# Optimization experiments

Hardware: AMD Instinct MI355X
Metric: run time of the kernel (lower is better)

The kernel has to match this reference:

```python
import jax, jax.numpy as jnp
import numpy as np

DIM = 512

def setup_inputs() -> dict:
    key = jax.random.key(0)
    ks = jax.random.split(key, 8)
    B, T, S, D = 4, 128, 512, DIM
    scale = 1.0 / np.sqrt(D)
    return {
        "inp": jax.random.normal(ks[0], (B, T, D), jnp.float32),
        "context": jax.random.normal(ks[1], (B, S, D), jnp.float32),
        # linear_query: Linear(D, D, bias=True)
        "Wq": jax.random.normal(ks[2], (D, D), jnp.float32) * scale,
        "bq": jax.random.normal(ks[3], (D,), jnp.float32) * scale,
        # linear_context: Linear(D, D, bias=False)
        "Wc": jax.random.normal(ks[4], (D, D), jnp.float32) * scale,
        # v: Linear(D, 1, bias=False)
        "v": jax.random.normal(ks[5], (D,), jnp.float32) * scale,
        # linear_out: Linear(2D, D, bias=True)
        "Wout": jax.random.normal(ks[6], (D, 2 * D), jnp.float32) * scale,
        "bout": jax.random.normal(ks[7], (D,), jnp.float32) * scale,
    }

def reference(inp, context, Wq, bq, Wc, v, Wout, bout):
    # inp: (B,T,D) target queries; context: (B,S,D) source states
    wq = jnp.einsum('btd,ed->bte', inp, Wq) + bq          # (B,T,D)
    uh = jnp.einsum('bsd,ed->bse', context, Wc)            # (B,S,D)
    # additive (Bahdanau) score: v^T tanh(Wq q_t + Wc h_s)
    wquh = jnp.tanh(wq[:, :, None, :] + uh[:, None, :, :])  # (B,T,S,D)
    align = jnp.einsum('btsd,d->bts', wquh, v)             # (B,T,S)
    align_vectors = jax.nn.softmax(align, axis=-1)          # softmax over src_len
    c = jnp.einsum('bts,bsd->btd', align_vectors, context)  # context vector
    concat_c = jnp.concatenate([c, inp], axis=-1)           # (B,T,2D)
    attn_h = jnp.einsum('btf,ef->bte', concat_c, Wout) + bout  # (B,T,D)
    return attn_h, align_vectors
```

## Files before the change

kernel.cpp:

```cpp
#include <hip/hip_runtime.h>
#include <hip/hip_bf16.h>
#include <math.h>


typedef __attribute__((ext_vector_type(8))) short short8;
typedef __attribute__((ext_vector_type(4))) float f32x4;
typedef unsigned short ushort_t;

static __device__ __forceinline__ unsigned short f2bf(float x) {
    union { __hip_bfloat16 h; unsigned short u; } c;
    c.h = __float2bfloat16(x);
    return c.u;
}
static __device__ __forceinline__ int bf2x(float lo, float hi) {
    return (int)(((unsigned)f2bf(hi) << 16) | (unsigned)f2bf(lo));
}

template<bool BF>
static __device__ __forceinline__ void load16(const void* base, size_t elemoff,
                                              int4& r0, int4& r1) {
    if (BF) {
        const int4* p = (const int4*)((const ushort_t*)base + elemoff);
        r0 = p[0]; r1 = p[1];
    } else {
        const float4* p = (const float4*)((const float*)base + elemoff);
        float4 a = p[0], b = p[1], c = p[2], d = p[3];
        r0.x = bf2x(a.x, a.y); r0.y = bf2x(a.z, a.w);
        r0.z = bf2x(b.x, b.y); r0.w = bf2x(b.z, b.w);
        r1.x = bf2x(c.x, c.y); r1.y = bf2x(c.z, c.w);
        r1.z = bf2x(d.x, d.y); r1.w = bf2x(d.z, d.w);
    }
}

template<bool A_BF, bool W_BF, int EPI>
static __device__ __forceinline__ void gemm_body(
    ushort_t* As, ushort_t* Ws,
    const void* A, const void* W, const float* bias, const float* partial,
    void* Cv, int K, int lda, int ldw, int ldc, int bm, int bn)
{
    const int tid = threadIdx.x;
    const int wave = tid >> 6, lane = tid & 63;
    const int mh = (wave & 1) * 32, nh = (wave >> 1) * 32;
    const int quad = lane >> 4, l16 = lane & 15;
    const int srow = tid >> 2, schunk = tid & 3;

    const size_t aoff = (size_t)(bm + srow) * lda + schunk * 16;
    const size_t woff = (size_t)(bn + srow) * ldw + schunk * 16;
    int4* AsW = (int4*)&As[srow * 72 + schunk * 16];
    int4* WsW = (int4*)&Ws[srow * 72 + schunk * 16];

    f32x4 acc00 = {0.f, 0.f, 0.f, 0.f}, acc01 = acc00, acc10 = acc00, acc11 = acc00;

    int4 a0r, a1r, w0r, w1r;
    load16<A_BF>(A, aoff, a0r, a1r);
    load16<W_BF>(W, woff, w0r, w1r);

    for (int k0 = 0; k0 < K; k0 += 64) {
        AsW[0] = a0r; AsW[1] = a1r;
        WsW[0] = w0r; WsW[1] = w1r;
        __syncthreads();
        if (k0 + 64 < K) {
            load16<A_BF>(A, aoff + k0 + 64, a0r, a1r);
            load16<W_BF>(W, woff + k0 + 64, w0r, w1r);
        }
        #pragma unroll
        for (int kk = 0; kk < 64; kk += 32) {
            short8 a0 = *(const short8*)&As[(mh + l16) * 72 + kk + quad * 8];
            short8 a1 = *(const short8*)&As[(mh + 16 + l16) * 72 + kk + quad * 8];
            short8 b0 = *(const short8*)&Ws[(nh + l16) * 72 + kk + quad * 8];
            short8 b1 = *(const short8*)&Ws[(nh + 16 + l16) * 72 + kk + quad * 8];
            acc00 = __builtin_amdgcn_mfma_f32_16x16x32_bf16(a0, b0, acc00, 0, 0, 0);
            acc01 = __builtin_amdgcn_mfma_f32_16x16x32_bf16(a0, b1, acc01, 0, 0, 0);
            acc10 = __builtin_amdgcn_mfma_f32_16x16x32_bf16(a1, b0, acc10, 0, 0, 0);
            acc11 = __builtin_amdgcn_mfma_f32_16x16x32_bf16(a1, b1, acc11, 0, 0, 0);
        }
        __syncthreads();
    }

    const int col0 = bn + nh + l16;
    const int col1 = col0 + 16;
    float bias0 = bias ? bias[col0] : 0.f;
    float bias1 = bias ? bias[col1] : 0.f;

    f32x4 accs[2][2] = {{acc00, acc01}, {acc10, acc11}};
    #pragma unroll
    for (int mt = 0; mt < 2; ++mt) {
        #pragma unroll
        for (int r = 0; r < 4; ++r) {
            int row = bm + mh + mt * 16 + quad * 4 + r;
            size_t rowoff = (size_t)row * ldc;
            float v0 = accs[mt][0][r] + bias0;
            float v1 = accs[mt][1][r] + bias1;
            if (EPI == 1) { v0 = __expf(2.f * v0); v1 = __expf(2.f * v1); }
            if (EPI == 3) { v0 += partial[rowoff + col0]; v1 += partial[rowoff + col1]; }
            if (EPI == 2) {
                ushort_t* C = (ushort_t*)Cv;
                C[rowoff + col0] = f2bf(v0);
                C[rowoff + col1] = f2bf(v1);
            } else {
                float* C = (float*)Cv;
                C[rowoff + col0] = v0;
                C[rowoff + col1] = v1;
            }
        }
    }
}

__global__ __launch_bounds__(256) void fused_front(
    const float* __restrict__ inp, const float* __restrict__ ctx,
    const float* __restrict__ Wq, const float* __restrict__ bq,
    const float* __restrict__ Wc, const float* __restrict__ Wout,
    const float* __restrict__ bout,
    float* __restrict__ Ew, float* __restrict__ Eu, float* __restrict__ Y0,
    ushort_t* __restrict__ GT)
{
    __shared__ ushort_t As[64 * 72];
    __shared__ ushort_t Ws[64 * 72];
    const int bid = blockIdx.x;

    if (bid < 64) {
        gemm_body<false, false, 1>(As, Ws, inp, Wq, bq, nullptr, Ew,
                                   512, 512, 512, 512, (bid & 7) * 64, (bid >> 3) * 64);
    } else if (bid < 320) {
        int i = bid - 64;
        gemm_body<false, false, 1>(As, Ws, ctx, Wc, nullptr, nullptr, Eu,
                                   512, 512, 512, 512, (i & 31) * 64, (i >> 5) * 64);
    } else if (bid < 576) {
        int i = bid - 320;
        int b = i >> 6, j = i & 63;
        gemm_body<false, false, 2>(As, Ws, Wout, ctx + (size_t)b * 262144, nullptr,
                                   nullptr, GT + (size_t)b * 262144,
                                   512, 1024, 512, 512, (j & 7) * 64, (j >> 3) * 64);
    } else {
        int i = bid - 576;
        gemm_body<false, false, 0>(As, Ws, inp, Wout + 512, bout, nullptr, Y0,
                                   512, 512, 1024, 512, (i & 7) * 64, (i >> 3) * 64);
    }
}

__global__ __launch_bounds__(256) void align_kernel(
    const float* __restrict__ Ew, const float* __restrict__ Eu,
    const float* __restrict__ v, float* __restrict__ out)
{
    const int lane = threadIdx.x & 63, wave = threadIdx.x >> 6;
    const int b = blockIdx.z;
    const int t0 = blockIdx.y * 16 + wave * 4;
    const int s0 = blockIdx.x * 8;

    const float* wp = Ew + (((size_t)(b * 128 + t0)) << 9);
    const float* up = Eu + (((size_t)(b * 512 + s0)) << 9);

    float acc[4][8];
    #pragma unroll
    for (int i = 0; i < 4; ++i)
        #pragma unroll
        for (int j = 0; j < 8; ++j) acc[i][j] = 0.f;
    float vsum = 0.f;

    for (int k0 = 0; k0 < 512; k0 += 64) {
        float vk = v[k0 + lane];
        vsum += vk;
        float w0 = wp[k0 + lane];
        float w1 = wp[512 + k0 + lane];
        float w2 = wp[1024 + k0 + lane];
        float w3 = wp[1536 + k0 + lane];
        #pragma unroll
        for (int j = 0; j < 8; ++j) {
            float u = up[((size_t)j << 9) + k0 + lane];
            float d0 = fmaf(w0, u, 1.f);
            float d1 = fmaf(w1, u, 1.f);
            float d2 = fmaf(w2, u, 1.f);
            float d3 = fmaf(w3, u, 1.f);
            float r0 = __builtin_amdgcn_rcpf(d0);
            float r1 = __builtin_amdgcn_rcpf(d1);
            float r2 = __builtin_amdgcn_rcpf(d2);
            float r3 = __builtin_amdgcn_rcpf(d3);
            acc[0][j] = fmaf(vk, r0, acc[0][j]);
            acc[1][j] = fmaf(vk, r1, acc[1][j]);
            acc[2][j] = fmaf(vk, r2, acc[2][j]);
            acc[3][j] = fmaf(vk, r3, acc[3][j]);
        }
    }

    float V = vsum;
    #pragma unroll
    for (int off = 32; off; off >>= 1) V += __shfl_xor(V, off, 64);

    float r0 = 0.f, r1 = 0.f, r2 = 0.f, r3 = 0.f;
    #pragma unroll
    for (int j = 0; j < 8; ++j) {
        float a0 = acc[0][j], a1 = acc[1][j], a2 = acc[2][j], a3 = acc[3][j];
        #pragma unroll
        for (int off = 32; off; off >>= 1) {
            a0 += __shfl_xor(a0, off, 64);
            a1 += __shfl_xor(a1, off, 64);
            a2 += __shfl_xor(a2, off, 64);
            a3 += __shfl_xor(a3, off, 64);
        }
        if (lane == j) {
            r0 = fmaf(-2.f, a0, V);
            r1 = fmaf(-2.f, a1, V);
            r2 = fmaf(-2.f, a2, V);
            r3 = fmaf(-2.f, a3, V);
        }
    }
    if (lane < 8) {
        size_t o = (((size_t)(b * 128 + t0)) << 9) + s0 + lane;
        out[o] = r0;
        out[o + 512] = r1;
        out[o + 1024] = r2;
        out[o + 1536] = r3;
    }
}

__global__ __launch_bounds__(256) void softmax_512(
    const float* __restrict__ Sraw, float* __restrict__ alignv,
    ushort_t* __restrict__ pbf)
{
    const int row = blockIdx.x;
    const float* p = Sraw + ((size_t)row << 9);
    float* a = alignv + ((size_t)row << 9);
    ushort_t* q = pbf + ((size_t)row << 9);
    const int tid = threadIdx.x;
    float x0 = p[tid];
    float x1 = p[tid + 256];

    float m = fmaxf(x0, x1);
    #pragma unroll
    for (int off = 32; off > 0; off >>= 1)
        m = fmaxf(m, __shfl_xor(m, off, 64));
    __shared__ float redm[4];
    __shared__ float reds[4];
    const int wave = tid >> 6;
    if ((tid & 63) == 0) redm[wave] = m;
    __syncthreads();
    m = fmaxf(fmaxf(redm[0], redm[1]), fmaxf(redm[2], redm[3]));

    float e0 = __expf(x0 - m);
    float e1 = __expf(x1 - m);
    float s = e0 + e1;
    #pragma unroll
    for (int off = 32; off > 0; off >>= 1)
        s += __shfl_xor(s, off, 64);
    if ((tid & 63) == 0) reds[wave] = s;
    __syncthreads();
    s = reds[0] + reds[1] + reds[2] + reds[3];
    float r = 1.0f / s;
    float p0 = e0 * r, p1 = e1 * r;
    a[tid] = p0;
    a[tid + 256] = p1;
    q[tid] = f2bf(p0);
    q[tid + 256] = f2bf(p1);
}

__global__ __launch_bounds__(256) void gemm_att(
    const ushort_t* __restrict__ P, const ushort_t* __restrict__ GT,
    const float* __restrict__ Y0, float* __restrict__ attn)
{
    __shared__ ushort_t As[64 * 72];
    __shared__ ushort_t Ws[64 * 72];
    const int b = blockIdx.z;
    gemm_body<true, true, 3>(As, Ws,
                             P + (size_t)b * 65536, GT + (size_t)b * 262144,
                             nullptr, Y0 + (size_t)b * 65536,
                             attn + (size_t)b * 65536,
                             512, 512, 512, 512, blockIdx.x * 64, blockIdx.y * 64);
}

extern "C" void kernel_launch(void* const* d_in, const int* in_sizes, int n_in,
                              void* d_out, int out_size, void* d_ws, size_t ws_size,
                              hipStream_t stream)
{
    const float* inp  = (const float*)d_in[0];
    const float* ctx  = (const float*)d_in[1];
    const float* Wq   = (const float*)d_in[2];
    const float* bq   = (const float*)d_in[3];
    const float* Wc   = (const float*)d_in[4];
    const float* v    = (const float*)d_in[5];
    const float* Wout = (const float*)d_in[6];
    const float* bout = (const float*)d_in[7];

    float* out    = (float*)d_out;
    float* attn   = out;
    float* alignv = out + 262144;

    float* ws = (float*)d_ws;
    float* Ew   = ws;
    float* Eu   = ws + 262144;
    float* Y0   = ws + 1310720;
    float* Sraw = ws + 1572864;
    ushort_t* GT   = (ushort_t*)(ws + 1835008);
    ushort_t* P_bf = (ushort_t*)(ws + 2359296);

    fused_front<<<dim3(640), 256, 0, stream>>>(inp, ctx, Wq, bq, Wc, Wout, bout,
                                               Ew, Eu, Y0, GT);
    align_kernel<<<dim3(64, 8, 4), 256, 0, stream>>>(Ew, Eu, v, Sraw);
    softmax_512<<<dim3(512), 256, 0, stream>>>(Sraw, alignv, P_bf);
    gemm_att<<<dim3(2, 8, 4), 256, 0, stream>>>(P_bf, GT, Y0, attn);
}
```

Baseline: 119.7 us.

## Fuse softmax into align and final GEMM using unnormalized exp with atomic row sums

Removes the separate softmax kernel. The align kernel now writes exp(score) directly and atomically adds per-row sums, with no max subtraction, which is safe because |score| is bounded by sum|v| via tanh. The final GEMM scales its A rows by 1/rowsum while loading and converting to bf16, and the blockIdx.y==0 blocks also write the normalized align vectors. This saves one launch and a round-trip of the score matrix, at the cost of atomics, an extra zeroing block in the front kernel, and fp32 reads of E instead of bf16 reads in the GEMM.

```diff
diff --git a/kernel.cpp b/kernel.cpp
--- a/kernel.cpp
+++ b/kernel.cpp
@@ -32,11 +32,26 @@
     }
 }
 
-template<bool A_BF, bool W_BF, int EPI>
+static __device__ __forceinline__ void load16s(const void* base, size_t elemoff,
+                                               float s, int4& r0, int4& r1) {
+    const float4* p = (const float4*)((const float*)base + elemoff);
+    float4 a = p[0], b = p[1], c = p[2], d = p[3];
+    a.x *= s; a.y *= s; a.z *= s; a.w *= s;
+    b.x *= s; b.y *= s; b.z *= s; b.w *= s;
+    c.x *= s; c.y *= s; c.z *= s; c.w *= s;
+    d.x *= s; d.y *= s; d.z *= s; d.w *= s;
+    r0.x = bf2x(a.x, a.y); r0.y = bf2x(a.z, a.w);
+    r0.z = bf2x(b.x, b.y); r0.w = bf2x(b.z, b.w);
+    r1.x = bf2x(c.x, c.y); r1.y = bf2x(c.z, c.w);
+    r1.z = bf2x(d.x, d.y); r1.w = bf2x(d.z, d.w);
+}
+
+template<bool A_BF, bool W_BF, int EPI, bool A_SCALE = false>
 static __device__ __forceinline__ void gemm_body(
     ushort_t* As, ushort_t* Ws,
     const void* A, const void* W, const float* bias, const float* partial,
-    void* Cv, int K, int lda, int ldw, int ldc, int bm, int bn)
+    void* Cv, int K, int lda, int ldw, int ldc, int bm, int bn,
+    const float* ascale = nullptr)
 {
     const int tid = threadIdx.x;
     const int wave = tid >> 6, lane = tid & 63;
@@ -49,10 +64,13 @@
     int4* AsW = (int4*)&As[srow * 72 + schunk * 16];
     int4* WsW = (int4*)&Ws[srow * 72 + schunk * 16];
 
+    const float asc = A_SCALE ? ascale[srow] : 1.f;
+
     f32x4 acc00 = {0.f, 0.f, 0.f, 0.f}, acc01 = acc00, acc10 = acc00, acc11 = acc00;
 
     int4 a0r, a1r, w0r, w1r;
-    load16<A_BF>(A, aoff, a0r, a1r);
+    if (A_SCALE) load16s(A, aoff, asc, a0r, a1r);
+    else         load16<A_BF>(A, aoff, a0r, a1r);
     load16<W_BF>(W, woff, w0r, w1r);
 
     for (int k0 = 0; k0 < K; k0 += 64) {
@@ -60,7 +78,8 @@
         WsW[0] = w0r; WsW[1] = w1r;
         __syncthreads();
         if (k0 + 64 < K) {
-            load16<A_BF>(A, aoff + k0 + 64, a0r, a1r);
+            if (A_SCALE) load16s(A, aoff + k0 + 64, asc, a0r, a1r);
+            else         load16<A_BF>(A, aoff + k0 + 64, a0r, a1r);
             load16<W_BF>(W, woff + k0 + 64, w0r, w1r);
         }
         #pragma unroll
@@ -112,11 +131,18 @@
     const float* __restrict__ Wc, const float* __restrict__ Wout,
     const float* __restrict__ bout,
     float* __restrict__ Ew, float* __restrict__ Eu, float* __restrict__ Y0,
-    ushort_t* __restrict__ GT)
+    ushort_t* __restrict__ GT, float* __restrict__ rowsum)
 {
     __shared__ ushort_t As[64 * 72];
     __shared__ ushort_t Ws[64 * 72];
     const int bid = blockIdx.x;
+
+    if (bid >= 640) {
+        float4 z = {0.f, 0.f, 0.f, 0.f};
+        ((float4*)rowsum)[threadIdx.x * 2]     = z;
+        ((float4*)rowsum)[threadIdx.x * 2 + 1] = z;
+        return;
+    }
 
     if (bid < 64) {
         gemm_body<false, false, 1>(As, Ws, inp, Wq, bq, nullptr, Ew,
@@ -138,9 +164,10 @@
     }
 }
 
-__global__ __launch_bounds__(256) void align_kernel(
+__global__ __launch_bounds__(256) void align_exp(
     const float* __restrict__ Ew, const float* __restrict__ Eu,
-    const float* __restrict__ v, float* __restrict__ out)
+    const float* __restrict__ v, float* __restrict__ out,
+    float* __restrict__ rowsum)
 {
     const int lane = threadIdx.x & 63, wave = threadIdx.x >> 6;
     const int b = blockIdx.z;
@@ -204,67 +231,65 @@
             r3 = fmaf(-2.f, a3, V);
         }
     }
+
+    float e0 = 0.f, e1 = 0.f, e2 = 0.f, e3 = 0.f;
     if (lane < 8) {
+        e0 = __expf(r0); e1 = __expf(r1); e2 = __expf(r2); e3 = __expf(r3);
         size_t o = (((size_t)(b * 128 + t0)) << 9) + s0 + lane;
-        out[o] = r0;
-        out[o + 512] = r1;
-        out[o + 1024] = r2;
-        out[o + 1536] = r3;
-    }
-}
-
-__global__ __launch_bounds__(256) void softmax_512(
-    const float* __restrict__ Sraw, float* __restrict__ alignv,
-    ushort_t* __restrict__ pbf)
-{
-    const int row = blockIdx.x;
-    const float* p = Sraw + ((size_t)row << 9);
-    float* a = alignv + ((size_t)row << 9);
-    ushort_t* q = pbf + ((size_t)row << 9);
-    const int tid = threadIdx.x;
-    float x0 = p[tid];
-    float x1 = p[tid + 256];
-
-    float m = fmaxf(x0, x1);
-    #pragma unroll
-    for (int off = 32; off > 0; off >>= 1)
-        m = fmaxf(m, __shfl_xor(m, off, 64));
-    __shared__ float redm[4];
-    __shared__ float reds[4];
-    const int wave = tid >> 6;
-    if ((tid & 63) == 0) redm[wave] = m;
-    __syncthreads();
-    m = fmaxf(fmaxf(redm[0], redm[1]), fmaxf(redm[2], redm[3]));
-
-    float e0 = __expf(x0 - m);
-    float e1 = __expf(x1 - m);
-    float s = e0 + e1;
-    #pragma unroll
-    for (int off = 32; off > 0; off >>= 1)
-        s += __shfl_xor(s, off, 64);
-    if ((tid & 63) == 0) reds[wave] = s;
-    __syncthreads();
-    s = reds[0] + reds[1] + reds[2] + reds[3];
-    float r = 1.0f / s;
-    float p0 = e0 * r, p1 = e1 * r;
-    a[tid] = p0;
-    a[tid + 256] = p1;
-    q[tid] = f2bf(p0);
-    q[tid + 256] = f2bf(p1);
-}
-
-__global__ __launch_bounds__(256) void gemm_att(
-    const ushort_t* __restrict__ P, const ushort_t* __restrict__ GT,
-    const float* __restrict__ Y0, float* __restrict__ attn)
+        out[o] = e0;
+        out[o + 512] = e1;
+        out[o + 1024] = e2;
+        out[o + 1536] = e3;
+    }
+    #pragma unroll
+    for (int off = 4; off; off >>= 1) {
+        e0 += __shfl_xor(e0, off, 64);
+        e1 += __shfl_xor(e1, off, 64);
+        e2 += __shfl_xor(e2, off, 64);
+        e3 += __shfl_xor(e3, off, 64);
+    }
+    if (lane == 0) {
+        const int row = b * 128 + t0;
+        atomicAdd(&rowsum[row],     e0);
+        atomicAdd(&rowsum[row + 1], e1);
+        atomicAdd(&rowsum[row + 2], e2);
+        atomicAdd(&rowsum[row + 3], e3);
+    }
+}
+
+__global__ __launch_bounds__(256) void gemm_att_sm(
+    const float* __restrict__ E, const ushort_t* __restrict__ GT,
+    const float* __restrict__ Y0, const float* __restrict__ rowsum,
+    float* __restrict__ attn, float* __restrict__ alignv)
 {
     __shared__ ushort_t As[64 * 72];
     __shared__ ushort_t Ws[64 * 72];
+    __shared__ float rinv[64];
     const int b = blockIdx.z;
-    gemm_body<true, true, 3>(As, Ws,
-                             P + (size_t)b * 65536, GT + (size_t)b * 262144,
-                             nullptr, Y0 + (size_t)b * 65536,
-                             attn + (size_t)b * 65536,
-                             512, 512, 512, 512, blockIdx.x * 64, blockIdx.y * 64);
+    const int bm = blockIdx.x * 64;
+    const int tid = threadIdx.x;
+
+    if (tid < 64) rinv[tid] = 1.0f / rowsum[b * 128 + bm + tid];
+    __syncthreads();
+
+    gemm_body<false, true, 3, true>(As, Ws,
+                                    E + (size_t)b * 65536, GT + (size_t)b * 262144,
+                                    nullptr, Y0 + (size_t)b * 65536,
+                                    attn + (size_t)b * 65536,
+                                    512, 512, 512, 512, bm, blockIdx.y * 64, rinv);
+
+    if (blockIdx.y == 0) {
+        const float* Eb = E + (size_t)b * 65536;
+        float* av = alignv + (size_t)b * 65536;
+        for (int i = tid; i < 8192; i += 256) {
+            int r = i >> 7, c4 = i & 127;
+            const float4* src = (const float4*)(Eb + ((size_t)(bm + r) << 9));
+            float4 e = src[c4];
+            float s = rinv[r];
+            e.x *= s; e.y *= s; e.z *= s; e.w *= s;
+            ((float4*)(av + ((size_t)(bm + r) << 9)))[c4] = e;
+        }
+    }
 }
 
 extern "C" void kernel_launch(void* const* d_in, const int* in_sizes, int n_in,
@@ -288,13 +313,12 @@
     float* Ew   = ws;
     float* Eu   = ws + 262144;
     float* Y0   = ws + 1310720;
-    float* Sraw = ws + 1572864;
-    ushort_t* GT   = (ushort_t*)(ws + 1835008);
-    ushort_t* P_bf = (ushort_t*)(ws + 2359296);
-
-    fused_front<<<dim3(640), 256, 0, stream>>>(inp, ctx, Wq, bq, Wc, Wout, bout,
-                                               Ew, Eu, Y0, GT);
-    align_kernel<<<dim3(64, 8, 4), 256, 0, stream>>>(Ew, Eu, v, Sraw);
-    softmax_512<<<dim3(512), 256, 0, stream>>>(Sraw, alignv, P_bf);
-    gemm_att<<<dim3(2, 8, 4), 256, 0, stream>>>(P_bf, GT, Y0, attn);
-}
+    float* E    = ws + 1572864;
+    ushort_t* GT = (ushort_t*)(ws + 1835008);
+    float* rowsum = ws + 2359296;
+
+    fused_front<<<dim3(641), 256, 0, stream>>>(inp, ctx, Wq, bq, Wc, Wout, bout,
+                                               Ew, Eu, Y0, GT, rowsum);
+    align_exp<<<dim3(64, 8, 4), 256, 0, stream>>>(Ew, Eu, v, E, rowsum);
+    gemm_att_sm<<<dim3(2, 8, 4), 256, 0, stream>>>(E, GT, Y0, rowsum, attn, alignv);
+}
```

Result: slower. 173.0 us (+44.6%).

## Transpose context projection and pair reciprocals in align kernel

Applied to the files above, without the earlier changes.

The context projection is now written transposed (EuT, laid out [b][d][s]) so that in the align kernel each lane owns one source position and reads along s with coalesced loads. This removes the per-row cross-lane shuffle reductions. Terms are combined two at a time as (v0*B+v1*A)/(A*B), which halves the number of reciprocal instructions at the cost of a few extra multiplies. Risks include overflow or precision loss from multiplying denominators, and the Ew and v loads are now lane-uniform.

```diff
diff --git a/kernel.cpp b/kernel.cpp
--- a/kernel.cpp
+++ b/kernel.cpp
@@ -111,7 +111,7 @@
     const float* __restrict__ Wq, const float* __restrict__ bq,
     const float* __restrict__ Wc, const float* __restrict__ Wout,
     const float* __restrict__ bout,
-    float* __restrict__ Ew, float* __restrict__ Eu, float* __restrict__ Y0,
+    float* __restrict__ Ew, float* __restrict__ EuT, float* __restrict__ Y0,
     ushort_t* __restrict__ GT)
 {
     __shared__ ushort_t As[64 * 72];
@@ -123,8 +123,10 @@
                                    512, 512, 512, 512, (bid & 7) * 64, (bid >> 3) * 64);
     } else if (bid < 320) {
         int i = bid - 64;
-        gemm_body<false, false, 1>(As, Ws, ctx, Wc, nullptr, nullptr, Eu,
-                                   512, 512, 512, 512, (i & 31) * 64, (i >> 5) * 64);
+        int b = i >> 6, j = i & 63;
+        gemm_body<false, false, 1>(As, Ws, Wc, ctx + (size_t)b * 262144, nullptr,
+                                   nullptr, EuT + (size_t)b * 262144,
+                                   512, 512, 512, 512, (j & 7) * 64, (j >> 3) * 64);
     } else if (bid < 576) {
         int i = bid - 320;
         int b = i >> 6, j = i & 63;
@@ -139,78 +141,56 @@
 }
 
 __global__ __launch_bounds__(256) void align_kernel(
-    const float* __restrict__ Ew, const float* __restrict__ Eu,
+    const float* __restrict__ Ew, const float* __restrict__ EuT,
     const float* __restrict__ v, float* __restrict__ out)
 {
     const int lane = threadIdx.x & 63, wave = threadIdx.x >> 6;
     const int b = blockIdx.z;
-    const int t0 = blockIdx.y * 16 + wave * 4;
-    const int s0 = blockIdx.x * 8;
-
-    const float* wp = Ew + (((size_t)(b * 128 + t0)) << 9);
-    const float* up = Eu + (((size_t)(b * 512 + s0)) << 9);
-
-    float acc[4][8];
-    #pragma unroll
-    for (int i = 0; i < 4; ++i)
+    const int t = blockIdx.y * 4 + wave;
+    const int s = blockIdx.x * 64 + lane;
+
+    const float* wp = Ew + (((size_t)(b * 128 + t)) << 9);
+    const float* up = EuT + ((size_t)b << 18) + s;
+
+    float vv = 0.f;
+    #pragma unroll
+    for (int i = 0; i < 8; ++i) vv += v[lane + 64 * i];
+    #pragma unroll
+    for (int off = 32; off; off >>= 1) vv += __shfl_xor(vv, off, 64);
+
+    float acc0 = 0.f, acc1 = 0.f, acc2 = 0.f, acc3 = 0.f;
+
+    for (int k0 = 0; k0 < 512; k0 += 8) {
+        float w_[8], v_[8], u_[8];
         #pragma unroll
-        for (int j = 0; j < 8; ++j) acc[i][j] = 0.f;
-    float vsum = 0.f;
-
-    for (int k0 = 0; k0 < 512; k0 += 64) {
-        float vk = v[k0 + lane];
-        vsum += vk;
-        float w0 = wp[k0 + lane];
-        float w1 = wp[512 + k0 + lane];
-        float w2 = wp[1024 + k0 + lane];
-        float w3 = wp[1536 + k0 + lane];
-        #pragma unroll
-        for (int j = 0; j < 8; ++j) {
-            float u = up[((size_t)j << 9) + k0 + lane];
-            float d0 = fmaf(w0, u, 1.f);
-            float d1 = fmaf(w1, u, 1.f);
-            float d2 = fmaf(w2, u, 1.f);
-            float d3 = fmaf(w3, u, 1.f);
-            float r0 = __builtin_amdgcn_rcpf(d0);
-            float r1 = __builtin_amdgcn_rcpf(d1);
-            float r2 = __builtin_amdgcn_rcpf(d2);
-            float r3 = __builtin_amdgcn_rcpf(d3);
-            acc[0][j] = fmaf(vk, r0, acc[0][j]);
-            acc[1][j] = fmaf(vk, r1, acc[1][j]);
-            acc[2][j] = fmaf(vk, r2, acc[2][j]);
-            acc[3][j] = fmaf(vk, r3, acc[3][j]);
-        }
-    }
-
-    float V = vsum;
-    #pragma unroll
-    for (int off = 32; off; off >>= 1) V += __shfl_xor(V, off, 64);
-
-    float r0 = 0.f, r1 = 0.f, r2 = 0.f, r3 = 0.f;
-    #pragma unroll
-    for (int j = 0; j < 8; ++j) {
-        float a0 = acc[0][j], a1 = acc[1][j], a2 = acc[2][j], a3 = acc[3][j];
-        #pragma unroll
-        for (int off = 32; off; off >>= 1) {
-            a0 += __shfl_xor(a0, off, 64);
-            a1 += __shfl_xor(a1, off, 64);
-            a2 += __shfl_xor(a2, off, 64);
-            a3 += __shfl_xor(a3, off, 64);
-        }
-        if (lane == j) {
-            r0 = fmaf(-2.f, a0, V);
-            r1 = fmaf(-2.f, a1, V);
-            r2 = fmaf(-2.f, a2, V);
-            r3 = fmaf(-2.f, a3, V);
-        }
-    }
-    if (lane < 8) {
-        size_t o = (((size_t)(b * 128 + t0)) << 9) + s0 + lane;
-        out[o] = r0;
-        out[o + 512] = r1;
-        out[o + 1024] = r2;
-        out[o + 1536] = r3;
-    }
+        for (int i = 0; i < 8; ++i) {
+            w_[i] = wp[k0 + i];
+            v_[i] = v[k0 + i];
+            u_[i] = up[(size_t)(k0 + i) << 9];
+        }
+        float A0 = fmaf(w_[0], u_[0], 1.f);
+        float B0 = fmaf(w_[1], u_[1], 1.f);
+        float n0 = fmaf(v_[0], B0, v_[1] * A0);
+        acc0 = fmaf(n0, __builtin_amdgcn_rcpf(A0 * B0), acc0);
+
+        float A1 = fmaf(w_[2], u_[2], 1.f);
+        float B1 = fmaf(w_[3], u_[3], 1.f);
+        float n1 = fmaf(v_[2], B1, v_[3] * A1);
+        acc1 = fmaf(n1, __builtin_amdgcn_rcpf(A1 * B1), acc1);
+
+        float A2 = fmaf(w_[4], u_[4], 1.f);
+        float B2 = fmaf(w_[5], u_[5], 1.f);
+        float n2 = fmaf(v_[4], B2, v_[5] * A2);
+        acc2 = fmaf(n2, __builtin_amdgcn_rcpf(A2 * B2), acc2);
+
+        float A3 = fmaf(w_[6], u_[6], 1.f);
+        float B3 = fmaf(w_[7], u_[7], 1.f);
+        float n3 = fmaf(v_[6], B3, v_[7] * A3);
+        acc3 = fmaf(n3, __builtin_amdgcn_rcpf(A3 * B3), acc3);
+    }
+
+    float acc = (acc0 + acc1) + (acc2 + acc3);
+    out[(((size_t)(b * 128 + t)) << 9) + s] = fmaf(-2.f, acc, vv);
 }
 
 __global__ __launch_bounds__(256) void softmax_512(
@@ -286,15 +266,15 @@
 
     float* ws = (float*)d_ws;
     float* Ew   = ws;
-    float* Eu   = ws + 262144;
+    float* EuT  = ws + 262144;
     float* Y0   = ws + 1310720;
     float* Sraw = ws + 1572864;
     ushort_t* GT   = (ushort_t*)(ws + 1835008);
     ushort_t* P_bf = (ushort_t*)(ws + 2359296);
 
     fused_front<<<dim3(640), 256, 0, stream>>>(inp, ctx, Wq, bq, Wc, Wout, bout,
-                                               Ew, Eu, Y0, GT);
-    align_kernel<<<dim3(64, 8, 4), 256, 0, stream>>>(Ew, Eu, v, Sraw);
+                                               Ew, EuT, Y0, GT);
+    align_kernel<<<dim3(8, 32, 4), 256, 0, stream>>>(Ew, EuT, v, Sraw);
     softmax_512<<<dim3(512), 256, 0, stream>>>(Sraw, alignv, P_bf);
     gemm_att<<<dim3(2, 8, 4), 256, 0, stream>>>(P_bf, GT, Y0, attn);
 }
```

Result: slower. 133.0 us (+11.1%).
